# Optimization experiments

Hardware: AMD Instinct MI355X
Metric: run time of the kernel (lower is better)

## Reference

```python
import jax, jax.numpy as jnp
import numpy as np

V0, V1 = 0.1, 0.2  # SSD encode/decode variances
LEVEL_WS = [160, 80, 40, 20, 10, 5]
BOUNDS = [0, 25600, 32000, 33600, 34000, 34100, 34125]
A_TOTAL = 34125
CLS_W, LOC_W = 1.0, 2.0

def _to_cxcywh(a):
    return np.stack([(a[:, 0] + a[:, 2]) / 2.0, (a[:, 1] + a[:, 3]) / 2.0,
                     a[:, 2] - a[:, 0], a[:, 3] - a[:, 1]], 1)

def _decode(d, anc):
    xy = anc[:, :2] + d[:, :2] * V0 * anc[:, 2:]
    wh = anc[:, 2:] * np.exp(d[:, 2:] * V1)
    return np.concatenate([xy - wh / 2.0, xy + wh / 2.0], 1)

def _encode(anc, gt):
    gcx = (gt[:, 0] + gt[:, 2]) / 2.0; gcy = (gt[:, 1] + gt[:, 3]) / 2.0
    gw = gt[:, 2] - gt[:, 0]; gh = gt[:, 3] - gt[:, 1]
    return np.stack([(gcx - anc[:, 0]) / (anc[:, 2] * V0),
                     (gcy - anc[:, 1]) / (anc[:, 3] * V0),
                     np.log(np.maximum(gw, 1e-6) / anc[:, 2]) / V1,
                     np.log(np.maximum(gh, 1e-6) / anc[:, 3]) / V1], 1)

def _relabel(conf, bbox_targets, anchors):
    # Faithful mirror of the torch.no_grad() relabel loop: per-image per-level
    # decode, unique-with-counts, center-distance top-k, sigmoid-score sort,
    # scatter relabel. Data-dependent shapes, so done in numpy (no grads flow here).
    conf = np.asarray(conf); bt = np.array(bbox_targets, copy=True); anc = np.asarray(anchors)
    tanc = _to_cxcywh(anc)
    labels = bt[:, :, -1].copy()
    for b in range(conf.shape[0]):
        pos = bt[b, :, -1] == 1
        uniq = []
        for li in range(6):
            s, e = BOUNDS[li], BOUNDS[li + 1]
            m = pos[s:e]
            dec = _decode(bt[b, s:e][m][:, :4], tanc[s:e][m])
            uniq.append(np.unique(np.round(dec, 3), axis=0, return_counts=True))
        start_idx, end_idx, tmp_w = -25600, 0, 160.0
        for li, (u, c) in enumerate(uniq):
            if li > 4:
                continue
            if u.shape[0] == 0:
                continue
            max_num = int(c.max())
            start_idx += int(tmp_w ** 2); end_idx += int(tmp_w ** 2); tmp_w /= 2.0
            s, e = start_idx, end_idx
            ctr = tanc[s:e, :2]
            for ti in range(u.shape[0]):
                n_match = int(c[ti])
                if n_match == max_num:
                    continue
                gt = u[ti]
                dist = np.hypot(ctr[:, 0] - (gt[0] + gt[2]) / 2.0, ctr[:, 1] - (gt[1] + gt[3]) / 2.0)
                cand = np.argsort(dist, kind='stable')[:max_num]
                scores = 1.0 / (1.0 + np.exp(-conf[b, s + cand, 0]))
                order = np.argsort(scores, kind='stable')
                rel = cand[order[-(max_num - n_match):]] + s
                rel = rel[labels[b, rel] != 1]
                if rel.shape[0] == 0:
                    continue
                bt[b, rel, :4] = _encode(tanc[rel], np.repeat(gt[None, :], rel.shape[0], 0))
                bt[b, rel, 4] = 1.0
                labels[b, rel] = 1.0
    return labels.astype(np.float32), bt.astype(np.float32)

def _losses(conf, loc, labels, bt):
    # cls: sigmoid BCE-with-logits summed, normalized by num positives
    # loc: smooth-L1 on encoded deltas over positive anchors, same normalization
    tgt = (labels == 1).astype(conf.dtype)
    z = conf[..., 0]
    bce = jnp.maximum(z, 0) - z * tgt + jnp.log1p(jnp.exp(-jnp.abs(z)))
    num_pos = jnp.maximum(tgt.sum(), 1.0)
    cls_loss = CLS_W * bce.sum() / num_pos
    d = loc - bt[..., :4]
    sl1 = jnp.where(jnp.abs(d) < 1.0, 0.5 * d * d, jnp.abs(d) - 0.5)
    loc_loss = LOC_W * (sl1 * tgt[..., None]).sum() / num_pos
    return cls_loss, loc_loss, cls_loss + loc_loss

def setup_inputs() -> dict:
    rng = np.random.RandomState(0)
    B, NGT = 16, 8
    anchors = []
    for w in LEVEL_WS:
        stride = 640.0 / w
        t = (np.arange(w) + 0.5) * stride
        cy, cx = np.meshgrid(t, t, indexing='ij')
        cx = cx.reshape(-1); cy = cy.reshape(-1); sz = 4.0 * stride
        anchors.append(np.stack([cx - sz / 2, cy - sz / 2, cx + sz / 2, cy + sz / 2], 1))
    anchors = np.concatenate(anchors, 0).astype(np.float32)  # [34125, 4]
    tanc = _to_cxcywh(anchors)
    bt = np.zeros((B, A_TOTAL, 5), np.float32)
    bt[:, :, :4] = rng.randn(B, A_TOTAL, 4).astype(np.float32) * 0.1
    gts = np.zeros((B, NGT, 4), np.float32)
    for b in range(B):
        for g in range(NGT):
            cx, cy = rng.uniform(64, 576, 2); sz = rng.uniform(16, 256)
            gt = np.array([cx - sz / 2, cy - sz / 2, cx + sz / 2, cy + sz / 2], np.float32)
            gts[b, g] = gt
            li = int(rng.randint(0, 5))
            s, e = BOUNDS[li], BOUNDS[li + 1]
            k = int(rng.randint(2, 20))
            idx = rng.choice(e - s, size=k, replace=False) + s
            bt[b, idx, :4] = _encode(tanc[idx], np.repeat(gt[None, :], k, 0)).astype(np.float32)
            bt[b, idx, 4] = 1.0
    conf = rng.randn(B, A_TOTAL, 1).astype(np.float32)
    loc = (rng.randn(B, A_TOTAL, 4) * 0.1).astype(np.float32)
    return {"conf": jnp.asarray(conf), "loc": jnp.asarray(loc),
            "bbox_targets": jnp.asarray(bt), "anchors": jnp.asarray(anchors),
            "bbox_labels_list": jnp.asarray(gts)}

def reference(conf, loc, bbox_targets, anchors, bbox_labels_list):
    labels, bt = _relabel(conf, bbox_targets, anchors)
    return _losses(conf, loc, jnp.asarray(labels), jnp.asarray(bt))
```

## Files before the change

### kernel.cpp

```cpp
#include <hip/hip_runtime.h>
#include <cstdint>
#include <cstddef>

#define A_TOTAL 34125
#define BATCH 16
#define NBA (BATCH * A_TOTAL)
#define SBT 1024
#define PT2 25
#define NB 1024
#define CAND 768
#define NSEG (BATCH * 5)
#define NSEG6 (BATCH * 6)
#define CCAP 16384
#define SELGRID 160

__device__ __constant__ int d_bounds[7] = {0, 25600, 32000, 33600, 34000, 34100, 34125};

#define MAXU 48
#define MAXPOS 512
#define MAXC 32
#define CLAIM_NONE 0x7FFFFFFF

__global__ __launch_bounds__(1024)
void setup_kernel(const float* __restrict__ bt,
                  const float* __restrict__ anchors,
                  const float* __restrict__ conf,
                  const float* __restrict__ loc,
                  int* __restrict__ claim,
                  float* __restrict__ part,
                  int* __restrict__ ccnt,
                  float2* __restrict__ ctr,
                  float* __restrict__ uq,
                  int* __restrict__ uc,
                  int* __restrict__ nu_out,
                  int* __restrict__ mn_out,
                  int* __restrict__ wl,
                  int* __restrict__ wlc)
{
    const int tid = threadIdx.x;
    const int gtid = blockIdx.x * blockDim.x + tid;
    const int gsz = gridDim.x * blockDim.x;
    if (gtid == 0) *ccnt = 0;

    int4* c4 = (int4*)claim;
    const int n4 = NBA / 4;
    for (int i = gtid; i < n4; i += gsz)
        c4[i] = make_int4(CLAIM_NONE, CLAIM_NONE, CLAIM_NONE, CLAIM_NONE);
    for (int a = gtid; a < A_TOTAL; a += gsz) {
        const float4 ar = reinterpret_cast<const float4*>(anchors)[a];
        ctr[a] = make_float2((ar.x + ar.z) / 2.0f, (ar.y + ar.w) / 2.0f);
    }

    float bce = 0.0f, pos = 0.0f, l1 = 0.0f;

    const float4* cf4 = (const float4*)conf;
    for (int i = gtid; i < NBA / 4; i += gsz) {
        const float4 z4 = cf4[i];
        const float zz[4] = {z4.x, z4.y, z4.z, z4.w};
        #pragma unroll
        for (int c = 0; c < 4; ++c) {
            const float z = zz[c];
            bce += fmaxf(z, 0.0f) + log1pf(expf(-fabsf(z)));
        }
    }

    const int b = blockIdx.x / 6;
    const int lv = blockIdx.x % 6;
    const unsigned bA = (unsigned)b * A_TOTAL;

    __shared__ int s_pos[MAXPOS];
    __shared__ float t0[MAXPOS], t1[MAXPOS], t2[MAXPOS], t3[MAXPOS];
    __shared__ int s_cnt[MAXPOS];
    __shared__ uint8_t s_rep[MAXPOS];
    __shared__ int s_ucs[MAXU];
    __shared__ int s_np, s_nu;

    if (tid == 0) { s_np = 0; s_nu = 0; }
    __syncthreads();

    {
        const unsigned fstart = (bA + d_bounds[lv]) * 5u;
        const unsigned fend   = (bA + d_bounds[lv + 1]) * 5u;
        const unsigned astart = (fstart + 3u) & ~3u;
        const unsigned aend   = fend & ~3u;
        for (unsigned g = fstart + tid; g < astart; g += blockDim.x)
            if (g % 5u == 4u && bt[g] == 1.0f) {
                int p = atomicAdd(&s_np, 1);
                if (p < MAXPOS) s_pos[p] = (int)(g / 5u - bA);
            }
        for (unsigned g = aend + tid; g < fend; g += blockDim.x)
            if (g % 5u == 4u && bt[g] == 1.0f) {
                int p = atomicAdd(&s_np, 1);
                if (p < MAXPOS) s_pos[p] = (int)(g / 5u - bA);
            }
        const float4* btv = (const float4*)bt;
        for (unsigned f4 = astart / 4u + tid; f4 < aend / 4u; f4 += blockDim.x) {
            const float4 v = btv[f4];
            const unsigned g0 = f4 * 4u;
            const unsigned m = g0 % 5u;
            if (m != 0u) {
                const unsigned c = 4u - m;
                const float val = (c == 0u) ? v.x : (c == 1u) ? v.y : (c == 2u) ? v.z : v.w;
                if (val == 1.0f) {
                    int p = atomicAdd(&s_np, 1);
                    if (p < MAXPOS) s_pos[p] = (int)((g0 + c) / 5u - bA);
                }
            }
        }
    }
    __syncthreads();
    const int np_ = min(s_np, MAXPOS);

    for (int p = tid; p < np_; p += blockDim.x) {
        const unsigned idx = bA + (unsigned)s_pos[p];
        bce -= conf[idx];
        pos += 1.0f;
        const unsigned row = idx * 5u;
        const float4 lvv = reinterpret_cast<const float4*>(loc)[idx];
        const float dv[4] = {lvv.x - bt[row], lvv.y - bt[row + 1],
                             lvv.z - bt[row + 2], lvv.w - bt[row + 3]};
        #pragma unroll
        for (int c = 0; c < 4; ++c) {
            const float ad = fabsf(dv[c]);
            l1 += (ad < 1.0f) ? 0.5f * dv[c] * dv[c] : ad - 0.5f;
        }
    }

    if (lv < 5) {
        const int seg = b * 5 + lv;

        for (int p = tid; p < np_; p += blockDim.x) {
            int a = s_pos[p];
            const float* ar = anchors + (size_t)a * 4;
            float acx = (ar[0] + ar[2]) / 2.0f;
            float acy = (ar[1] + ar[3]) / 2.0f;
            float aw = ar[2] - ar[0];
            float ah = ar[3] - ar[1];
            const float* dd = bt + ((size_t)bA + a) * 5;
            float cx = acx + (dd[0] * 0.1f) * aw;
            float cy = acy + (dd[1] * 0.1f) * ah;
            float w = aw * expf(dd[2] * 0.2f);
            float h = ah * expf(dd[3] * 0.2f);
            t0[p] = rintf((cx - w / 2.0f) * 1000.0f) / 1000.0f;
            t1[p] = rintf((cy - h / 2.0f) * 1000.0f) / 1000.0f;
            t2[p] = rintf((cx + w / 2.0f) * 1000.0f) / 1000.0f;
            t3[p] = rintf((cy + h / 2.0f) * 1000.0f) / 1000.0f;
        }
        __syncthreads();

        for (int p = tid; p < np_; p += blockDim.x) {
            const float p0 = t0[p], p1 = t1[p], p2 = t2[p], p3 = t3[p];
            int cnt = 0, firstq = np_;
            for (int q = 0; q < np_; ++q) {
                bool eq = (t0[q] == p0) && (t1[q] == p1) && (t2[q] == p2) && (t3[q] == p3);
                if (eq) { cnt++; if (q < firstq) firstq = q; }
            }
            s_cnt[p] = cnt;
            bool rep = (firstq == p);
            s_rep[p] = rep ? 1 : 0;
            if (rep) atomicAdd(&s_nu, 1);
        }
        __syncthreads();

        float* uqp = uq + (size_t)seg * MAXU * 4;
        int* ucp = uc + (size_t)seg * MAXU;
        for (int p = tid; p < np_; p += blockDim.x) {
            if (!s_rep[p]) continue;
            const float p0 = t0[p], p1 = t1[p], p2 = t2[p], p3 = t3[p];
            int rank = 0;
            for (int q = 0; q < np_; ++q) {
                if (!s_rep[q]) continue;
                float q0 = t0[q], q1 = t1[q], q2 = t2[q], q3 = t3[q];
                bool lt = (q0 < p0) || (q0 == p0 && (q1 < p1 ||
                          (q1 == p1 && (q2 < p2 || (q2 == p2 && q3 < p3)))));
                if (lt) rank++;
            }
            if (rank < MAXU) {
                uqp[rank * 4 + 0] = p0; uqp[rank * 4 + 1] = p1;
                uqp[rank * 4 + 2] = p2; uqp[rank * 4 + 3] = p3;
                ucp[rank] = s_cnt[p];
                s_ucs[rank] = s_cnt[p];
            }
        }
        __syncthreads();

        if (tid == 0) {
            const int nu = min(s_nu, MAXU);
            nu_out[seg] = nu;
            int mn = 0;
            for (int j = 0; j < nu; ++j) mn = max(mn, s_ucs[j]);
            mn_out[seg] = mn;
            int n = 0;
            for (int ti = 0; ti < nu; ++ti)
                if (s_ucs[ti] != mn) wl[seg * MAXU + n++] = seg * MAXU + ti;
            wlc[seg] = n;
        }
    }

    for (int off = 32; off > 0; off >>= 1) {
        bce += __shfl_down(bce, off);
        pos += __shfl_down(pos, off);
        l1  += __shfl_down(l1, off);
    }
    __shared__ float sb[3][16];
    const int wid = tid >> 6, lane = tid & 63;
    if (lane == 0) { sb[0][wid] = bce; sb[1][wid] = pos; sb[2][wid] = l1; }
    __syncthreads();
    if (tid == 0) {
        float B = 0, P = 0, L = 0;
        #pragma unroll
        for (int w = 0; w < 16; ++w) { B += sb[0][w]; P += sb[1][w]; L += sb[2][w]; }
        part[blockIdx.x * 3 + 0] = B;
        part[blockIdx.x * 3 + 1] = P;
        part[blockIdx.x * 3 + 2] = L;
    }
}

__global__ __launch_bounds__(SBT)
void select_kernel(const float* __restrict__ conf,
                   const float2* __restrict__ ctr,
                   const float* __restrict__ uq,
                   const int* __restrict__ uc,
                   const int* __restrict__ nu_,
                   const int* __restrict__ mn_,
                   const int* __restrict__ wl,
                   const int* __restrict__ wlc,
                   int* __restrict__ claim,
                   int2* __restrict__ clist,
                   int* __restrict__ ccnt) {
    const int tid = threadIdx.x;

    __shared__ int s_hist[NB];
    __shared__ unsigned long long s_cand[CAND];
    __shared__ unsigned long long s_srt[MAXC];
    __shared__ float s_sc[MAXC];
    __shared__ int s_c, s_B;

    for (int w = blockIdx.x; ; w += gridDim.x) {
        int cum = 0, ent = -1;
        for (int i = 0; i < NSEG; ++i) {
            int c = wlc[i];
            if (ent < 0 && w < cum + c) ent = wl[i * MAXU + (w - cum)];
            cum += c;
        }
        if (w >= cum) return;

        const int ti = ent % MAXU;
        const int sg = ent / MAXU;
        const int li = sg % 5;
        const int b  = sg / 5;

        int nus[5];
        #pragma unroll
        for (int l = 0; l < 5; ++l) nus[l] = nu_[b * 5 + l];

        int s = -25600;
        float tmpw = 160.0f;
        for (int l = 0; l <= li; ++l) {
            if (nus[l] != 0) { s += (int)(tmpw * tmpw); tmpw *= 0.5f; }
        }

        const int mn = mn_[sg];
        const int cnt = uc[(size_t)sg * MAXU + ti];
        const int need = mn - cnt;
        const int K = min(mn, MAXC);
        const unsigned bA = (unsigned)b * A_TOTAL;

        const float* g = uq + ((size_t)sg * MAXU + ti) * 4;
        const float gcx = (g[0] + g[2]) / 2.0f;
        const float gcy = (g[1] + g[3]) / 2.0f;

        float cxr[PT2], cyr[PT2];
        #pragma unroll
        for (int i = 0; i < PT2; ++i) {
            const float2 c = ctr[s + tid + (i << 10)];
            cxr[i] = c.x;
            cyr[i] = c.y;
        }

        s_hist[tid] = 0;
        if (tid == 0) s_c = 0;
        __syncthreads();

        #pragma unroll
        for (int i = 0; i < PT2; ++i) {
            float d = hypotf(cxr[i] - gcx, cyr[i] - gcy);
            int bin = min(NB - 1, (int)d);
            atomicAdd(&s_hist[bin], 1);
        }
        __syncthreads();

        if (tid < 64) {
            const int base = tid << 4;
            int part[16], psum = 0;
            #pragma unroll
            for (int i = 0; i < 16; ++i) { part[i] = s_hist[base + i]; psum += part[i]; }
            int run = psum;
            #pragma unroll
            for (int off = 1; off < 64; off <<= 1) {
                int o = __shfl_up(run, off);
                if (tid >= off) run += o;
            }
            const int excl = run - psum;
            if (excl < K && excl + psum >= K) {
                int c = excl, bs = base + 15;
                for (int i = 0; i < 16; ++i) { c += part[i]; if (c >= K) { bs = base + i; break; } }
                s_B = bs;
            }
        }
        __syncthreads();
        const int B = s_B;

        #pragma unroll
        for (int i = 0; i < PT2; ++i) {
            float d = hypotf(cxr[i] - gcx, cyr[i] - gcy);
            int bin = min(NB - 1, (int)d);
            if (bin <= B) {
                int p = atomicAdd(&s_c, 1);
                if (p < CAND)
                    s_cand[p] = (((unsigned long long)__float_as_uint(d)) << 32) |
                                (unsigned)(tid + (i << 10));
            }
        }
        __syncthreads();
        const int C = min(s_c, CAND);

        if (tid < C) {
            const unsigned long long mykey = s_cand[tid];
            int rank = 0;
            for (int j = 0; j < C; ++j) rank += (s_cand[j] < mykey) ? 1 : 0;
            if (rank < K) s_srt[rank] = mykey;
        }
        __syncthreads();

        if (tid < K) {
            const int o = (int)(s_srt[tid] & 0xffffffffULL);
            const float z = conf[bA + s + o];
            s_sc[tid] = 1.0f / (1.0f + expf(-z));
        }
        __syncthreads();

        if (tid < K) {
            const float my = s_sc[tid];
            int r = 0;
            for (int j = 0; j < K; ++j) {
                const float oj = s_sc[j];
                r += (oj > my || (oj == my && j > tid)) ? 1 : 0;
            }
            if (r < need) {
                const int o = (int)(s_srt[tid] & 0xffffffffULL);
                const int idx = (int)(bA + s + o);
                const int seq = li * MAXU + ti;
                atomicMin(&claim[idx], seq);
                int p = atomicAdd(ccnt, 1);
                if (p < CCAP) clist[p] = make_int2(idx, seq);
            }
        }
        __syncthreads();
    }
}

__global__ __launch_bounds__(1024)
void finalize_kernel(const float* __restrict__ conf,
                     const float* __restrict__ loc,
                     const float* __restrict__ bt,
                     const float* __restrict__ anchors,
                     const float* __restrict__ uq,
                     const int2* __restrict__ clist,
                     const int* __restrict__ ccnt,
                     const int* __restrict__ claim,
                     const float* __restrict__ part,
                     float* __restrict__ out) {
    const int tid = threadIdx.x;
    float bce = 0.0f, pos = 0.0f, l1 = 0.0f;
    const int cn = min(*ccnt, CCAP);
    for (int e = tid; e < cn; e += blockDim.x) {
        const int2 ent = clist[e];
        const int idx = ent.x;
        if (claim[idx] != ent.y) continue;
        if (bt[(size_t)idx * 5 + 4] == 1.0f) continue;
        bce -= conf[idx];
        pos += 1.0f;
        const int uli = ent.y / MAXU;
        const int uti = ent.y - uli * MAXU;
        const int b = idx / A_TOTAL;
        const int a = idx - b * A_TOTAL;
        const float* g = uq + ((size_t)(b * 5 + uli) * MAXU + uti) * 4;
        const float g0 = g[0], g1 = g[1], g2 = g[2], g3 = g[3];
        const float gcx = (g0 + g2) / 2.0f, gcy = (g1 + g3) / 2.0f;
        const float gw = g2 - g0, gh = g3 - g1;
        const float* ar = anchors + (size_t)a * 4;
        const float acx = (ar[0] + ar[2]) / 2.0f;
        const float acy = (ar[1] + ar[3]) / 2.0f;
        const float aw = ar[2] - ar[0];
        const float ah = ar[3] - ar[1];
        float ep[4];
        ep[0] = (gcx - acx) / (aw * 0.1f);
        ep[1] = (gcy - acy) / (ah * 0.1f);
        ep[2] = logf(fmaxf(gw, 1e-6f) / aw) / 0.2f;
        ep[3] = logf(fmaxf(gh, 1e-6f) / ah) / 0.2f;
        const float4 lvv = reinterpret_cast<const float4*>(loc)[idx];
        const float lvf[4] = {lvv.x, lvv.y, lvv.z, lvv.w};
        #pragma unroll
        for (int c = 0; c < 4; ++c) {
            const float dd = lvf[c] - ep[c];
            const float ad = fabsf(dd);
            l1 += (ad < 1.0f) ? 0.5f * dd * dd : ad - 0.5f;
        }
    }

    for (int off = 32; off > 0; off >>= 1) {
        bce += __shfl_down(bce, off);
        pos += __shfl_down(pos, off);
        l1  += __shfl_down(l1, off);
    }
    __shared__ float sb[3][16];
    const int wid = tid >> 6, lane = tid & 63;
    if (lane == 0) { sb[0][wid] = bce; sb[1][wid] = pos; sb[2][wid] = l1; }
    __syncthreads();
    if (tid == 0) {
        float B = 0, P = 0, L = 0;
        #pragma unroll
        for (int w = 0; w < 16; ++w) { B += sb[0][w]; P += sb[1][w]; L += sb[2][w]; }
        double a0 = (double)B, a1 = (double)P, a2 = (double)L;
        for (int i = 0; i < NSEG6; ++i) {
            a0 += (double)part[i * 3 + 0];
            a1 += (double)part[i * 3 + 1];
            a2 += (double)part[i * 3 + 2];
        }
        const double np_ = a1 > 1.0 ? a1 : 1.0;
        const double cls = a0 / np_;
        const double lcl = 2.0 * a2 / np_;
        out[0] = (float)cls;
        out[1] = (float)lcl;
        out[2] = (float)(cls + lcl);
    }
}

extern "C" void kernel_launch(void* const* d_in, const int* in_sizes, int n_in,
                              void* d_out, int out_size, void* d_ws, size_t ws_size,
                              hipStream_t stream) {
    const float* conf    = (const float*)d_in[0];
    const float* loc     = (const float*)d_in[1];
    const float* bt      = (const float*)d_in[2];
    const float* anchors = (const float*)d_in[3];
    float* out = (float*)d_out;

    char* ws = (char*)d_ws;
    size_t off = 0;
    int* ccnt       = (int*)(ws + off);    off += 64;
    float* part     = (float*)(ws + off);  off += (size_t)NSEG6 * 3 * sizeof(float);
    int* claim      = (int*)(ws + off);    off += (size_t)NBA * sizeof(int);
    float* uq       = (float*)(ws + off);  off += (size_t)NSEG * MAXU * 4 * sizeof(float);
    int* uc         = (int*)(ws + off);    off += (size_t)NSEG * MAXU * sizeof(int);
    int* nu_        = (int*)(ws + off);    off += (size_t)NSEG * sizeof(int);
    int* mn_        = (int*)(ws + off);    off += (size_t)NSEG * sizeof(int);
    int* wl         = (int*)(ws + off);    off += (size_t)NSEG * MAXU * sizeof(int);
    int* wlc        = (int*)(ws + off);    off += ((size_t)NSEG * sizeof(int) + 15) & ~15ull;
    int2* clist     = (int2*)(ws + off);   off += (size_t)CCAP * sizeof(int2);
    float2* ctr     = (float2*)(ws + off); off += (size_t)A_TOTAL * sizeof(float2);

    setup_kernel<<<NSEG6, 1024, 0, stream>>>(bt, anchors, conf, loc, claim, part,
                                             ccnt, ctr, uq, uc, nu_, mn_, wl, wlc);
    select_kernel<<<SELGRID, SBT, 0, stream>>>(conf, ctr, uq, uc, nu_, mn_, wl, wlc,
                                               claim, clist, ccnt);
    finalize_kernel<<<1, 1024, 0, stream>>>(conf, loc, bt, anchors, uq, clist, ccnt,
                                            claim, part, out);
}
```

Measured before the change: 63.48 us.

## Split setup into wide scan kernel and per-segment dedup kernel via posmap

Replaces the 96-block, 1024-thread setup kernel with a 1024-block streaming scan. The scan fills claim, computes BCE and positive smooth-L1 partial sums, and writes a byte posmap of positive anchors. A separate 80-block dedup kernel then reads the posmap instead of rescanning bbox_targets, and does the per-segment unique/rank work. This spreads the bandwidth-bound pass over many more CUs, but adds a kernel launch, a posmap write/read, and a finalize reduction over 1024 partials done in float rather than double.

```diff
diff --git a/kernel.cpp b/kernel.cpp
--- a/kernel.cpp
+++ b/kernel.cpp
@@ -10,9 +10,10 @@
 #define NB 1024
 #define CAND 768
 #define NSEG (BATCH * 5)
-#define NSEG6 (BATCH * 6)
 #define CCAP 16384
 #define SELGRID 160
+#define SCAN_GRID 1024
+#define SCAN_THR 256
 
 __device__ __constant__ int d_bounds[7] = {0, 25600, 32000, 33600, 34000, 34100, 34125};
 
@@ -21,15 +22,93 @@
 #define MAXC 32
 #define CLAIM_NONE 0x7FFFFFFF
 
-__global__ __launch_bounds__(1024)
-void setup_kernel(const float* __restrict__ bt,
+__global__ __launch_bounds__(SCAN_THR)
+void scan_kernel(const float* __restrict__ bt,
+                 const float* __restrict__ anchors,
+                 const float* __restrict__ conf,
+                 const float* __restrict__ loc,
+                 int* __restrict__ claim,
+                 uint8_t* __restrict__ posmap,
+                 float* __restrict__ part,
+                 int* __restrict__ ccnt,
+                 float2* __restrict__ ctr) {
+    const int tid = threadIdx.x;
+    const int gtid = blockIdx.x * blockDim.x + tid;
+    const int gsz = gridDim.x * blockDim.x;
+    if (gtid == 0) *ccnt = 0;
+
+    int4* c4 = (int4*)claim;
+    for (int i = gtid; i < NBA / 4; i += gsz)
+        c4[i] = make_int4(CLAIM_NONE, CLAIM_NONE, CLAIM_NONE, CLAIM_NONE);
+    for (int a = gtid; a < A_TOTAL; a += gsz) {
+        const float4 ar = reinterpret_cast<const float4*>(anchors)[a];
+        ctr[a] = make_float2((ar.x + ar.z) / 2.0f, (ar.y + ar.w) / 2.0f);
+    }
+
+    float bce = 0.0f, pos = 0.0f, l1 = 0.0f;
+
+    const float4* cf4 = (const float4*)conf;
+    for (int i = gtid; i < NBA / 4; i += gsz) {
+        const float4 z4 = cf4[i];
+        const float zz[4] = {z4.x, z4.y, z4.z, z4.w};
+        #pragma unroll
+        for (int c = 0; c < 4; ++c) {
+            const float z = zz[c];
+            bce += fmaxf(z, 0.0f) + log1pf(expf(-fabsf(z)));
+        }
+    }
+
+    const float4* btv = (const float4*)bt;
+    const int nchunk = NBA * 5 / 4;
+    for (int f4 = gtid; f4 < nchunk; f4 += gsz) {
+        const float4 v = btv[f4];
+        const unsigned g0 = (unsigned)f4 * 4u;
+        const unsigned m = g0 % 5u;
+        if (m != 0u) {
+            const unsigned c = 4u - m;
+            const float val = (c == 0u) ? v.x : (c == 1u) ? v.y : (c == 2u) ? v.z : v.w;
+            const unsigned i = (g0 + c) / 5u;
+            const bool p = (val == 1.0f);
+            posmap[i] = p ? 1 : 0;
+            if (p) {
+                bce -= conf[i];
+                pos += 1.0f;
+                const float* tp = bt + (size_t)i * 5u;
+                const float4 lv4 = reinterpret_cast<const float4*>(loc)[i];
+                const float dv[4] = {lv4.x - tp[0], lv4.y - tp[1],
+                                     lv4.z - tp[2], lv4.w - tp[3]};
+                #pragma unroll
+                for (int cc = 0; cc < 4; ++cc) {
+                    const float ad = fabsf(dv[cc]);
+                    l1 += (ad < 1.0f) ? 0.5f * dv[cc] * dv[cc] : ad - 0.5f;
+                }
+            }
+        }
+    }
+
+    for (int off = 32; off > 0; off >>= 1) {
+        bce += __shfl_down(bce, off);
+        pos += __shfl_down(pos, off);
+        l1  += __shfl_down(l1, off);
+    }
+    __shared__ float sb[3][4];
+    const int wid = tid >> 6, lane = tid & 63;
+    if (lane == 0) { sb[0][wid] = bce; sb[1][wid] = pos; sb[2][wid] = l1; }
+    __syncthreads();
+    if (tid == 0) {
+        float B = 0, P = 0, L = 0;
+        #pragma unroll
+        for (int w = 0; w < 4; ++w) { B += sb[0][w]; P += sb[1][w]; L += sb[2][w]; }
+        part[blockIdx.x * 3 + 0] = B;
+        part[blockIdx.x * 3 + 1] = P;
+        part[blockIdx.x * 3 + 2] = L;
+    }
+}
+
+__global__ __launch_bounds__(256)
+void dedup_kernel(const float* __restrict__ bt,
                   const float* __restrict__ anchors,
-                  const float* __restrict__ conf,
-                  const float* __restrict__ loc,
-                  int* __restrict__ claim,
-                  float* __restrict__ part,
-                  int* __restrict__ ccnt,
-                  float2* __restrict__ ctr,
+                  const uint8_t* __restrict__ posmap,
                   float* __restrict__ uq,
                   int* __restrict__ uc,
                   int* __restrict__ nu_out,
@@ -37,36 +116,11 @@
                   int* __restrict__ wl,
                   int* __restrict__ wlc)
 {
+    const int b = blockIdx.x / 5;
+    const int lv = blockIdx.x % 5;
+    const int seg = blockIdx.x;
+    const unsigned bA = (unsigned)b * A_TOTAL;
     const int tid = threadIdx.x;
-    const int gtid = blockIdx.x * blockDim.x + tid;
-    const int gsz = gridDim.x * blockDim.x;
-    if (gtid == 0) *ccnt = 0;
-
-    int4* c4 = (int4*)claim;
-    const int n4 = NBA / 4;
-    for (int i = gtid; i < n4; i += gsz)
-        c4[i] = make_int4(CLAIM_NONE, CLAIM_NONE, CLAIM_NONE, CLAIM_NONE);
-    for (int a = gtid; a < A_TOTAL; a += gsz) {
-        const float4 ar = reinterpret_cast<const float4*>(anchors)[a];
-        ctr[a] = make_float2((ar.x + ar.z) / 2.0f, (ar.y + ar.w) / 2.0f);
-    }
-
-    float bce = 0.0f, pos = 0.0f, l1 = 0.0f;
-
-    const float4* cf4 = (const float4*)conf;
-    for (int i = gtid; i < NBA / 4; i += gsz) {
-        const float4 z4 = cf4[i];
-        const float zz[4] = {z4.x, z4.y, z4.z, z4.w};
-        #pragma unroll
-        for (int c = 0; c < 4; ++c) {
-            const float z = zz[c];
-            bce += fmaxf(z, 0.0f) + log1pf(expf(-fabsf(z)));
-        }
-    }
-
-    const int b = blockIdx.x / 6;
-    const int lv = blockIdx.x % 6;
-    const unsigned bA = (unsigned)b * A_TOTAL;
 
     __shared__ int s_pos[MAXPOS];
     __shared__ float t0[MAXPOS], t1[MAXPOS], t2[MAXPOS], t3[MAXPOS];
@@ -78,141 +132,80 @@
     if (tid == 0) { s_np = 0; s_nu = 0; }
     __syncthreads();
 
-    {
-        const unsigned fstart = (bA + d_bounds[lv]) * 5u;
-        const unsigned fend   = (bA + d_bounds[lv + 1]) * 5u;
-        const unsigned astart = (fstart + 3u) & ~3u;
-        const unsigned aend   = fend & ~3u;
-        for (unsigned g = fstart + tid; g < astart; g += blockDim.x)
-            if (g % 5u == 4u && bt[g] == 1.0f) {
-                int p = atomicAdd(&s_np, 1);
-                if (p < MAXPOS) s_pos[p] = (int)(g / 5u - bA);
-            }
-        for (unsigned g = aend + tid; g < fend; g += blockDim.x)
-            if (g % 5u == 4u && bt[g] == 1.0f) {
-                int p = atomicAdd(&s_np, 1);
-                if (p < MAXPOS) s_pos[p] = (int)(g / 5u - bA);
-            }
-        const float4* btv = (const float4*)bt;
-        for (unsigned f4 = astart / 4u + tid; f4 < aend / 4u; f4 += blockDim.x) {
-            const float4 v = btv[f4];
-            const unsigned g0 = f4 * 4u;
-            const unsigned m = g0 % 5u;
-            if (m != 0u) {
-                const unsigned c = 4u - m;
-                const float val = (c == 0u) ? v.x : (c == 1u) ? v.y : (c == 2u) ? v.z : v.w;
-                if (val == 1.0f) {
-                    int p = atomicAdd(&s_np, 1);
-                    if (p < MAXPOS) s_pos[p] = (int)((g0 + c) / 5u - bA);
-                }
-            }
+    for (int a = d_bounds[lv] + tid; a < d_bounds[lv + 1]; a += blockDim.x) {
+        if (posmap[bA + a]) {
+            int p = atomicAdd(&s_np, 1);
+            if (p < MAXPOS) s_pos[p] = a;
         }
     }
     __syncthreads();
     const int np_ = min(s_np, MAXPOS);
 
     for (int p = tid; p < np_; p += blockDim.x) {
-        const unsigned idx = bA + (unsigned)s_pos[p];
-        bce -= conf[idx];
-        pos += 1.0f;
-        const unsigned row = idx * 5u;
-        const float4 lvv = reinterpret_cast<const float4*>(loc)[idx];
-        const float dv[4] = {lvv.x - bt[row], lvv.y - bt[row + 1],
-                             lvv.z - bt[row + 2], lvv.w - bt[row + 3]};
-        #pragma unroll
-        for (int c = 0; c < 4; ++c) {
-            const float ad = fabsf(dv[c]);
-            l1 += (ad < 1.0f) ? 0.5f * dv[c] * dv[c] : ad - 0.5f;
-        }
-    }
-
-    if (lv < 5) {
-        const int seg = b * 5 + lv;
-
-        for (int p = tid; p < np_; p += blockDim.x) {
-            int a = s_pos[p];
-            const float* ar = anchors + (size_t)a * 4;
-            float acx = (ar[0] + ar[2]) / 2.0f;
-            float acy = (ar[1] + ar[3]) / 2.0f;
-            float aw = ar[2] - ar[0];
-            float ah = ar[3] - ar[1];
-            const float* dd = bt + ((size_t)bA + a) * 5;
-            float cx = acx + (dd[0] * 0.1f) * aw;
-            float cy = acy + (dd[1] * 0.1f) * ah;
-            float w = aw * expf(dd[2] * 0.2f);
-            float h = ah * expf(dd[3] * 0.2f);
-            t0[p] = rintf((cx - w / 2.0f) * 1000.0f) / 1000.0f;
-            t1[p] = rintf((cy - h / 2.0f) * 1000.0f) / 1000.0f;
-            t2[p] = rintf((cx + w / 2.0f) * 1000.0f) / 1000.0f;
-            t3[p] = rintf((cy + h / 2.0f) * 1000.0f) / 1000.0f;
-        }
-        __syncthreads();
-
-        for (int p = tid; p < np_; p += blockDim.x) {
-            const float p0 = t0[p], p1 = t1[p], p2 = t2[p], p3 = t3[p];
-            int cnt = 0, firstq = np_;
-            for (int q = 0; q < np_; ++q) {
-                bool eq = (t0[q] == p0) && (t1[q] == p1) && (t2[q] == p2) && (t3[q] == p3);
-                if (eq) { cnt++; if (q < firstq) firstq = q; }
-            }
-            s_cnt[p] = cnt;
-            bool rep = (firstq == p);
-            s_rep[p] = rep ? 1 : 0;
-            if (rep) atomicAdd(&s_nu, 1);
-        }
-        __syncthreads();
-
-        float* uqp = uq + (size_t)seg * MAXU * 4;
-        int* ucp = uc + (size_t)seg * MAXU;
-        for (int p = tid; p < np_; p += blockDim.x) {
-            if (!s_rep[p]) continue;
-            const float p0 = t0[p], p1 = t1[p], p2 = t2[p], p3 = t3[p];
-            int rank = 0;
-            for (int q = 0; q < np_; ++q) {
-                if (!s_rep[q]) continue;
-                float q0 = t0[q], q1 = t1[q], q2 = t2[q], q3 = t3[q];
-                bool lt = (q0 < p0) || (q0 == p0 && (q1 < p1 ||
-                          (q1 == p1 && (q2 < p2 || (q2 == p2 && q3 < p3)))));
-                if (lt) rank++;
-            }
-            if (rank < MAXU) {
-                uqp[rank * 4 + 0] = p0; uqp[rank * 4 + 1] = p1;
-                uqp[rank * 4 + 2] = p2; uqp[rank * 4 + 3] = p3;
-                ucp[rank] = s_cnt[p];
-                s_ucs[rank] = s_cnt[p];
-            }
-        }
-        __syncthreads();
-
-        if (tid == 0) {
-            const int nu = min(s_nu, MAXU);
-            nu_out[seg] = nu;
-            int mn = 0;
-            for (int j = 0; j < nu; ++j) mn = max(mn, s_ucs[j]);
-            mn_out[seg] = mn;
-            int n = 0;
-            for (int ti = 0; ti < nu; ++ti)
-                if (s_ucs[ti] != mn) wl[seg * MAXU + n++] = seg * MAXU + ti;
-            wlc[seg] = n;
-        }
-    }
-
-    for (int off = 32; off > 0; off >>= 1) {
-        bce += __shfl_down(bce, off);
-        pos += __shfl_down(pos, off);
-        l1  += __shfl_down(l1, off);
-    }
-    __shared__ float sb[3][16];
-    const int wid = tid >> 6, lane = tid & 63;
-    if (lane == 0) { sb[0][wid] = bce; sb[1][wid] = pos; sb[2][wid] = l1; }
-    __syncthreads();
+        int a = s_pos[p];
+        const float* ar = anchors + (size_t)a * 4;
+        float acx = (ar[0] + ar[2]) / 2.0f;
+        float acy = (ar[1] + ar[3]) / 2.0f;
+        float aw = ar[2] - ar[0];
+        float ah = ar[3] - ar[1];
+        const float* dd = bt + ((size_t)bA + a) * 5;
+        float cx = acx + (dd[0] * 0.1f) * aw;
+        float cy = acy + (dd[1] * 0.1f) * ah;
+        float w = aw * expf(dd[2] * 0.2f);
+        float h = ah * expf(dd[3] * 0.2f);
+        t0[p] = rintf((cx - w / 2.0f) * 1000.0f) / 1000.0f;
+        t1[p] = rintf((cy - h / 2.0f) * 1000.0f) / 1000.0f;
+        t2[p] = rintf((cx + w / 2.0f) * 1000.0f) / 1000.0f;
+        t3[p] = rintf((cy + h / 2.0f) * 1000.0f) / 1000.0f;
+    }
+    __syncthreads();
+
+    for (int p = tid; p < np_; p += blockDim.x) {
+        const float p0 = t0[p], p1 = t1[p], p2 = t2[p], p3 = t3[p];
+        int cnt = 0, firstq = np_;
+        for (int q = 0; q < np_; ++q) {
+            bool eq = (t0[q] == p0) && (t1[q] == p1) && (t2[q] == p2) && (t3[q] == p3);
+            if (eq) { cnt++; if (q < firstq) firstq = q; }
+        }
+        s_cnt[p] = cnt;
+        bool rep = (firstq == p);
+        s_rep[p] = rep ? 1 : 0;
+        if (rep) atomicAdd(&s_nu, 1);
+    }
+    __syncthreads();
+
+    float* uqp = uq + (size_t)seg * MAXU * 4;
+    int* ucp = uc + (size_t)seg * MAXU;
+    for (int p = tid; p < np_; p += blockDim.x) {
+        if (!s_rep[p]) continue;
+        const float p0 = t0[p], p1 = t1[p], p2 = t2[p], p3 = t3[p];
+        int rank = 0;
+        for (int q = 0; q < np_; ++q) {
+            if (!s_rep[q]) continue;
+            float q0 = t0[q], q1 = t1[q], q2 = t2[q], q3 = t3[q];
+            bool lt = (q0 < p0) || (q0 == p0 && (q1 < p1 ||
+                      (q1 == p1 && (q2 < p2 || (q2 == p2 && q3 < p3)))));
+            if (lt) rank++;
+        }
+        if (rank < MAXU) {
+            uqp[rank * 4 + 0] = p0; uqp[rank * 4 + 1] = p1;
+            uqp[rank * 4 + 2] = p2; uqp[rank * 4 + 3] = p3;
+            ucp[rank] = s_cnt[p];
+            s_ucs[rank] = s_cnt[p];
+        }
+    }
+    __syncthreads();
+
     if (tid == 0) {
-        float B = 0, P = 0, L = 0;
-        #pragma unroll
-        for (int w = 0; w < 16; ++w) { B += sb[0][w]; P += sb[1][w]; L += sb[2][w]; }
-        part[blockIdx.x * 3 + 0] = B;
-        part[blockIdx.x * 3 + 1] = P;
-        part[blockIdx.x * 3 + 2] = L;
+        const int nu = min(s_nu, MAXU);
+        nu_out[seg] = nu;
+        int mn = 0;
+        for (int j = 0; j < nu; ++j) mn = max(mn, s_ucs[j]);
+        mn_out[seg] = mn;
+        int n = 0;
+        for (int ti = 0; ti < nu; ++ti)
+            if (s_ucs[ti] != mn) wl[seg * MAXU + n++] = seg * MAXU + ti;
+        wlc[seg] = n;
     }
 }
 
@@ -409,6 +402,12 @@
         }
     }
 
+    if (tid < SCAN_GRID) {
+        bce += part[tid * 3 + 0];
+        pos += part[tid * 3 + 1];
+        l1  += part[tid * 3 + 2];
+    }
+
     for (int off = 32; off > 0; off >>= 1) {
         bce += __shfl_down(bce, off);
         pos += __shfl_down(pos, off);
@@ -422,12 +421,9 @@
         float B = 0, P = 0, L = 0;
         #pragma unroll
         for (int w = 0; w < 16; ++w) { B += sb[0][w]; P += sb[1][w]; L += sb[2][w]; }
-        double a0 = (double)B, a1 = (double)P, a2 = (double)L;
-        for (int i = 0; i < NSEG6; ++i) {
-            a0 += (double)part[i * 3 + 0];
-            a1 += (double)part[i * 3 + 1];
-            a2 += (double)part[i * 3 + 2];
-        }
+        const double a0 = (double)B;
+        const double a1 = (double)P;
+        const double a2 = (double)L;
         const double np_ = a1 > 1.0 ? a1 : 1.0;
         const double cls = a0 / np_;
         const double lcl = 2.0 * a2 / np_;
@@ -449,8 +445,9 @@
     char* ws = (char*)d_ws;
     size_t off = 0;
     int* ccnt       = (int*)(ws + off);    off += 64;
-    float* part     = (float*)(ws + off);  off += (size_t)NSEG6 * 3 * sizeof(float);
+    float* part     = (float*)(ws + off);  off += (size_t)SCAN_GRID * 3 * sizeof(float);
     int* claim      = (int*)(ws + off);    off += (size_t)NBA * sizeof(int);
+    uint8_t* posmap = (uint8_t*)(ws + off); off += ((size_t)NBA + 63) & ~63ull;
     float* uq       = (float*)(ws + off);  off += (size_t)NSEG * MAXU * 4 * sizeof(float);
     int* uc         = (int*)(ws + off);    off += (size_t)NSEG * MAXU * sizeof(int);
     int* nu_        = (int*)(ws + off);    off += (size_t)NSEG * sizeof(int);
@@ -460,8 +457,10 @@
     int2* clist     = (int2*)(ws + off);   off += (size_t)CCAP * sizeof(int2);
     float2* ctr     = (float2*)(ws + off); off += (size_t)A_TOTAL * sizeof(float2);
 
-    setup_kernel<<<NSEG6, 1024, 0, stream>>>(bt, anchors, conf, loc, claim, part,
-                                             ccnt, ctr, uq, uc, nu_, mn_, wl, wlc);
+    scan_kernel<<<SCAN_GRID, SCAN_THR, 0, stream>>>(bt, anchors, conf, loc, claim,
+                                                    posmap, part, ccnt, ctr);
+    dedup_kernel<<<NSEG, 256, 0, stream>>>(bt, anchors, posmap, uq, uc, nu_, mn_,
+                                           wl, wlc);
     select_kernel<<<SELGRID, SBT, 0, stream>>>(conf, ctr, uq, uc, nu_, mn_, wl, wlc,
                                                claim, clist, ccnt);
     finalize_kernel<<<1, 1024, 0, stream>>>(conf, loc, bt, anchors, uq, clist, ccnt,
```

Result: slower. 75.80 us (+19.4%).
